# Kernel optimization log

Measured on AMD Instinct MI355X. Metric: run time of the kernel, lower is better.

The kernel has to match this reference:

```python
import jax, jax.numpy as jnp
import numpy as np

NUM_USERS = 100000
NUM_ITEMS = 50000
EMB_DIM = 64
NUM_EDGES = 2000000


def setup_inputs() -> dict:
    key = jax.random.key(0)
    k1, k2, k3, k4 = jax.random.split(key, 4)
    user_table = jax.random.normal(k1, (NUM_USERS, EMB_DIM), dtype=jnp.float32) * 0.1
    item_table = jax.random.normal(k2, (NUM_ITEMS, EMB_DIM), dtype=jnp.float32) * 0.1
    user_idx = jax.random.randint(k3, (NUM_EDGES,), 0, NUM_USERS, dtype=jnp.int32)
    item_idx = jax.random.randint(k4, (NUM_EDGES,), 0, NUM_ITEMS, dtype=jnp.int32)
    return {"user_table": user_table, "item_table": item_table,
            "user_idx": user_idx, "item_idx": item_idx, "num_layers": 3}


def reference(user_table, item_table, user_idx, item_idx, num_layers):
    """LightGCN-style k-hop propagation over a sparse bipartite user-item graph.

    A_hat[u,i] = 1/sqrt(deg_u * deg_i); emb_out = mean over hops 0..K of A_hat^k @ emb_0.
    Returns concatenated [num_users+num_items, d] embeddings (forward() then slices).
    """
    n_users, d = user_table.shape
    n_items = item_table.shape[0]
    ones = jnp.ones(user_idx.shape[0], dtype=user_table.dtype)
    deg_u = jax.ops.segment_sum(ones, user_idx, num_segments=n_users)
    deg_i = jax.ops.segment_sum(ones, item_idx, num_segments=n_items)
    deg_u = jnp.where(deg_u > 0, deg_u, 1.0)
    deg_i = jnp.where(deg_i > 0, deg_i, 1.0)
    # per-edge symmetric normalization coefficient [E]
    norm = jax.lax.rsqrt(deg_u[user_idx] * deg_i[item_idx])

    u, it = user_table, item_table
    acc_u, acc_i = u, it
    for _ in range(num_layers):
        # messages: item -> user and user -> item (gather + weighted scatter-add)
        msg_u = jax.ops.segment_sum(norm[:, None] * it[item_idx], user_idx, num_segments=n_users)
        msg_i = jax.ops.segment_sum(norm[:, None] * u[user_idx], item_idx, num_segments=n_items)
        u, it = msg_u, msg_i
        acc_u = acc_u + u
        acc_i = acc_i + it
    scale = 1.0 / (num_layers + 1)
    return jnp.concatenate([acc_u * scale, acc_i * scale], axis=0)
```

## Files before the change

### kernel.cpp

```cpp
#include <hip/hip_runtime.h>
#include <hip/hip_fp16.h>
#include <stdint.h>

#define NU 100000
#define NI 50000
#define NN (NU + NI)
#define DIM 64
#define NE 2000000
#define TOT (NN * DIM)

#define NBU 782
#define NBI 782
#define NBKT (NBU + NBI)
#define SCAP 3064
#define CGRP 25
#define NC 63
#define CCAP 67584

#define BEPT1 4
#define BCH1 (256 * BEPT1)
#define BG1 ((NE + BCH1 - 1) / BCH1)
#define KB2 17

typedef float f4v __attribute__((ext_vector_type(4)));
typedef float f2v __attribute__((ext_vector_type(2)));

__device__ __forceinline__ int bucket_r0(int b) {
    return (b < NBU) ? (b << 7) : (NU + ((b - NBU) << 6));
}


__global__ void bin1_kernel(const int* __restrict__ uidx, const int* __restrict__ iidx,
                            int* __restrict__ ccur, uint32_t* __restrict__ cstg) {
    __shared__ int cnt[NC];
    __shared__ int base[NC + 1];
    __shared__ int gbase[NC];
    __shared__ uint32_t rec[2 * BCH1];
    __shared__ uint8_t cid[2 * BCH1];
    int tid = threadIdx.x;
    for (int i = tid; i < NC; i += 256) cnt[i] = 0;
    __syncthreads();

    uint32_t pk[2 * BEPT1]; int cs[2 * BEPT1]; int rk[2 * BEPT1];
    int t0 = blockIdx.x * BCH1 + tid;
#pragma unroll
    for (int k = 0; k < BEPT1; ++k) {
        int e = t0 + k * 256;
        bool ok = e < NE;
        int u = ok ? __builtin_nontemporal_load(uidx + e) : 0;
        int itm = ok ? __builtin_nontemporal_load(iidx + e) : 0;
        int b = u >> 7; int c = b / 25; int f5 = b - c * 25;
        pk[2 * k] = ((uint32_t)f5 << 23) | ((uint32_t)(u & 127) << 16) | (uint32_t)itm;
        cs[2 * k] = ok ? c : -1;
        int b2 = NBU + (itm >> 6); int c2 = b2 / 25; int f52 = b2 - c2 * 25;
        pk[2 * k + 1] = ((uint32_t)f52 << 23) | ((uint32_t)(itm & 63) << 17) | (uint32_t)u;
        cs[2 * k + 1] = ok ? c2 : -1;
    }
#pragma unroll
    for (int k = 0; k < 2 * BEPT1; ++k)
        rk[k] = (cs[k] >= 0) ? atomicAdd(&cnt[cs[k]], 1) : 0;
    __syncthreads();
    if (tid == 0) {
        int s = 0;
        for (int i = 0; i < NC; ++i) { base[i] = s; s += cnt[i]; }
        base[NC] = s;
    }
    __syncthreads();
    for (int i = tid; i < NC; i += 256)
        if (cnt[i] > 0) gbase[i] = atomicAdd(&ccur[i], cnt[i]);
#pragma unroll
    for (int k = 0; k < 2 * BEPT1; ++k)
        if (cs[k] >= 0) {
            int p = base[cs[k]] + rk[k];
            rec[p] = pk[k];
            cid[p] = (uint8_t)cs[k];
        }
    __syncthreads();
    int T = base[NC];
    for (int p = tid; p < T; p += 256) {
        int c = cid[p];
        int pos = gbase[c] + (p - base[c]);
        if (pos < CCAP)
            __builtin_nontemporal_store(rec[p], cstg + (size_t)c * CCAP + pos);
    }
}

__global__ void bin2_kernel(const int* __restrict__ ccnt, const uint32_t* __restrict__ cstg,
                            int* __restrict__ bktcur, uint32_t* __restrict__ stg) {
    int c = blockIdx.x / KB2;
    int sl = blockIdx.x % KB2;
    int n = min(ccnt[c], CCAP);
    int lo = sl * 4096;
    if (lo >= n) return;
    int hi = min(lo + 4096, n);
    int m = hi - lo;
    __shared__ int cnt[CGRP];
    __shared__ int base[CGRP + 1];
    __shared__ int gbase[CGRP];
    __shared__ uint32_t rec[4096];
    int tid = threadIdx.x;
    if (tid < CGRP) cnt[tid] = 0;
    __syncthreads();

    uint32_t pk[16]; int fa[16]; int rk[16];
    const uint32_t* run = cstg + (size_t)c * CCAP + lo;
#pragma unroll
    for (int k = 0; k < 16; ++k) {
        int p = tid + k * 256;
        bool ok = p < m;
        uint32_t r = ok ? __builtin_nontemporal_load(run + p) : 0;
        pk[k] = r;
        fa[k] = ok ? (int)(r >> 23) : -1;
    }
#pragma unroll
    for (int k = 0; k < 16; ++k)
        rk[k] = (fa[k] >= 0) ? atomicAdd(&cnt[fa[k]], 1) : 0;
    __syncthreads();
    if (tid == 0) {
        int s = 0;
        for (int i = 0; i < CGRP; ++i) { base[i] = s; s += cnt[i]; }
        base[CGRP] = s;
    }
    __syncthreads();
    if (tid < CGRP && cnt[tid] > 0)
        gbase[tid] = atomicAdd(&bktcur[c * CGRP + tid], cnt[tid]);
#pragma unroll
    for (int k = 0; k < 16; ++k)
        if (fa[k] >= 0) rec[base[fa[k]] + rk[k]] = pk[k];
    __syncthreads();
    int T = base[CGRP];
    for (int p = tid; p < T; p += 256) {
        uint32_t r = rec[p];
        int f5 = r >> 23;
        int pos = gbase[f5] + (p - base[f5]);
        if (pos < SCAP)
            __builtin_nontemporal_store(r, stg + (size_t)(c * CGRP + f5) * SCAP + pos);
    }
}

__global__ void scanB_kernel(const int* __restrict__ bktcnt, int* __restrict__ bktbase) {
    __shared__ int partial[256];
    int tid = threadIdx.x;
    int loc[7];
    int s = 0;
#pragma unroll
    for (int k = 0; k < 7; ++k) {
        int i = tid * 7 + k;
        loc[k] = (i < NBKT) ? min(bktcnt[i], SCAP) : 0;
        s += loc[k];
    }
    partial[tid] = s;
    __syncthreads();
    for (int off = 1; off < 256; off <<= 1) {
        int v = (tid >= off) ? partial[tid - off] : 0;
        __syncthreads();
        partial[tid] += v;
        __syncthreads();
    }
    int excl = (tid == 0) ? 0 : partial[tid - 1];
#pragma unroll
    for (int k = 0; k < 7; ++k) {
        int i = tid * 7 + k;
        if (i < NBKT) { bktbase[i] = excl; excl += loc[k]; }
    }
    if (tid == 255) bktbase[NBKT] = partial[255];
}

__global__ void placeB2_kernel(const int* __restrict__ bktbase, const uint32_t* __restrict__ stg,
                               int* __restrict__ rowptr, float* __restrict__ rdeg,
                               float* __restrict__ irdeg, int* __restrict__ nbrs) {
    __shared__ int rowstart[129];
    __shared__ int rowcnt[128];
    __shared__ int outb[SCAP];
    int b = blockIdx.x;
    int tid = threadIdx.x;
    int r0 = bucket_r0(b);
    int r1 = (b < NBU) ? min(r0 + 128, NU) : min(r0 + 64, NN);
    int nrows = r1 - r0;
    int lo = bktbase[b];
    int n = bktbase[b + 1] - lo;
    if (tid < nrows) rowcnt[tid] = 0;
    __syncthreads();
    const uint32_t* run = stg + (size_t)b * SCAP;
    bool isU = b < NBU;
    for (int p = tid; p < n; p += 256) {
        uint32_t r = __builtin_nontemporal_load(run + p);
        int row = isU ? ((r >> 16) & 0x7F) : ((r >> 17) & 0x3F);
        atomicAdd(&rowcnt[row], 1);
    }
    __syncthreads();
    if (tid == 0) {
        int s = 0;
        for (int i = 0; i < nrows; ++i) { rowstart[i] = s; s += rowcnt[i]; }
        rowstart[nrows] = s;
    }
    __syncthreads();
    if (tid < nrows) {
        int d = rowcnt[tid];
        rowptr[r0 + tid] = lo + rowstart[tid];
        rdeg[r0 + tid] = (d > 0) ? rsqrtf((float)d) : 1.0f;
        irdeg[r0 + tid] = (d > 0) ? sqrtf((float)d) : 1.0f;
        rowcnt[tid] = 0;
    }
    if (b == NBKT - 1 && tid == 0) rowptr[NN] = lo + n;
    __syncthreads();
    for (int p = tid; p < n; p += 256) {
        uint32_t r = __builtin_nontemporal_load(run + p);
        int row = isU ? ((r >> 16) & 0x7F) : ((r >> 17) & 0x3F);
        int nbr = isU ? (NU + (int)(r & 0xFFFF)) : (int)(r & 0x1FFFF);
        int rk = atomicAdd(&rowcnt[row], 1);
        outb[rowstart[row] + rk] = nbr;
    }
    __syncthreads();
    for (int i = tid; i < n; i += 256)
        __builtin_nontemporal_store(outb[i], nbrs + lo + i);
}


__global__ void initsrc_kernel(const float* __restrict__ ut, const float* __restrict__ it,
                               const float* __restrict__ rdeg, __half* __restrict__ srcH) {
    int i = blockIdx.x * blockDim.x + threadIdx.x;
    const int NU4 = NU * DIM / 4;
    const int T4 = TOT / 4;
    if (i >= T4) return;
    float4 v = (i < NU4) ? ((const float4*)ut)[i] : ((const float4*)it)[i - NU4];
    float r = rdeg[i >> 4];
    union { __half2 h2[2]; f2v v2; } u;
    u.h2[0] = __floats2half2_rn(r * v.x, r * v.y);
    u.h2[1] = __floats2half2_rn(r * v.z, r * v.w);
    *((f2v*)(srcH + (size_t)i * 4)) = u.v2;
}

__device__ __forceinline__ void gather_core(const int* __restrict__ rowptr,
                                            const int* __restrict__ nbrs,
                                            const __half* __restrict__ srcH,
                                            int wid, int lane, int g, int c,
                                            float* out) {
    int start = rowptr[wid];
    int end = rowptr[wid + 1];
    int deg = end - start;
    int nb_l = (lane < deg) ? __builtin_nontemporal_load(nbrs + start + lane) : 0;
    float acc[4][8];
#pragma unroll
    for (int j = 0; j < 4; ++j)
#pragma unroll
        for (int k = 0; k < 8; ++k) acc[j][k] = 0.f;
    int dmain = deg < 64 ? deg : 64;
    int iters = (dmain + 7) >> 3;
    int t = 0;
    for (; t + 4 <= iters; t += 4) {
        int nb[4]; bool ok[4];
#pragma unroll
        for (int j = 0; j < 4; ++j) {
            int idx = (t + j) * 8 + g;
            nb[j] = __shfl(nb_l, idx & 63, 64);
            ok[j] = idx < dmain;
            if (!ok[j]) nb[j] = 0;
        }
        union { f4v v; __half2 h2[4]; } u[4];
#pragma unroll
        for (int j = 0; j < 4; ++j)
            u[j].v = *((const f4v*)(srcH + (size_t)nb[j] * DIM) + c);
#pragma unroll
        for (int j = 0; j < 4; ++j)
            if (ok[j]) {
#pragma unroll
                for (int h = 0; h < 4; ++h) {
                    float2 f = __half22float2(u[j].h2[h]);
                    acc[j][2 * h] += f.x; acc[j][2 * h + 1] += f.y;
                }
            }
    }
    if (t + 2 <= iters) {
        int nb[2]; bool ok[2];
#pragma unroll
        for (int j = 0; j < 2; ++j) {
            int idx = (t + j) * 8 + g;
            nb[j] = __shfl(nb_l, idx & 63, 64);
            ok[j] = idx < dmain;
            if (!ok[j]) nb[j] = 0;
        }
        union { f4v v; __half2 h2[4]; } u[2];
#pragma unroll
        for (int j = 0; j < 2; ++j)
            u[j].v = *((const f4v*)(srcH + (size_t)nb[j] * DIM) + c);
#pragma unroll
        for (int j = 0; j < 2; ++j)
            if (ok[j]) {
#pragma unroll
                for (int h = 0; h < 4; ++h) {
                    float2 f = __half22float2(u[j].h2[h]);
                    acc[j][2 * h] += f.x; acc[j][2 * h + 1] += f.y;
                }
            }
        t += 2;
    }
    if (t < iters) {
        int idx = t * 8 + g;
        int nb0 = __shfl(nb_l, idx & 63, 64);
        bool ok0 = idx < dmain;
        if (!ok0) nb0 = 0;
        union { f4v v; __half2 h2[4]; } u0;
        u0.v = *((const f4v*)(srcH + (size_t)nb0 * DIM) + c);
        if (ok0) {
#pragma unroll
            for (int h = 0; h < 4; ++h) {
                float2 f = __half22float2(u0.h2[h]);
                acc[0][2 * h] += f.x; acc[0][2 * h + 1] += f.y;
            }
        }
    }
    for (int k = start + 64 + g; k < end; k += 8) {
        int nb = nbrs[k];
        union { f4v v; __half2 h2[4]; } u0;
        u0.v = *((const f4v*)(srcH + (size_t)nb * DIM) + c);
#pragma unroll
        for (int h = 0; h < 4; ++h) {
            float2 f = __half22float2(u0.h2[h]);
            acc[0][2 * h] += f.x; acc[0][2 * h + 1] += f.y;
        }
    }
    float s[8];
#pragma unroll
    for (int k = 0; k < 8; ++k)
        s[k] = acc[0][k] + acc[1][k] + acc[2][k] + acc[3][k];
#pragma unroll
    for (int mask = 8; mask <= 32; mask <<= 1) {
#pragma unroll
        for (int k = 0; k < 8; ++k) s[k] += __shfl_xor(s[k], mask, 64);
    }
#pragma unroll
    for (int k = 0; k < 8; ++k) out[k] = s[k];
}

__global__ void gather_kernel(const int* __restrict__ rowptr, const int* __restrict__ nbrs,
                              const float* __restrict__ rdeg,
                              const __half* __restrict__ srcH, __half* __restrict__ nxtH) {
    int wid = (int)(((unsigned)blockIdx.x * blockDim.x + threadIdx.x) >> 6);
    if (wid >= NN) return;
    int lane = threadIdx.x & 63;
    int g = lane >> 3;
    int c = lane & 7;
    float s[8];
    gather_core(rowptr, nbrs, srcH, wid, lane, g, c, s);
    if (lane < 8) {
        float r = rdeg[wid];
        float w = r * r;
        union { f4v v; __half2 h2[4]; } o;
        o.h2[0] = __floats2half2_rn(w * s[0], w * s[1]);
        o.h2[1] = __floats2half2_rn(w * s[2], w * s[3]);
        o.h2[2] = __floats2half2_rn(w * s[4], w * s[5]);
        o.h2[3] = __floats2half2_rn(w * s[6], w * s[7]);
        __builtin_nontemporal_store(o.v, (f4v*)(nxtH + (size_t)wid * DIM + c * 8));
    }
}

__global__ void gather_fused_kernel(const int* __restrict__ rowptr, const int* __restrict__ nbrs,
                                    const float* __restrict__ rdeg, const float* __restrict__ irdeg,
                                    const __half* __restrict__ srcH,
                                    const __half* __restrict__ a0H, const __half* __restrict__ n1H,
                                    float* __restrict__ acc) {
    int wid = (int)(((unsigned)blockIdx.x * blockDim.x + threadIdx.x) >> 6);
    if (wid >= NN) return;
    int lane = threadIdx.x & 63;
    int g = lane >> 3;
    int c = lane & 7;
    float s[8];
    gather_core(rowptr, nbrs, srcH, wid, lane, g, c, s);
    if (lane < 8) {
        float r = rdeg[wid];
        float w = irdeg[wid];
        size_t ro = (size_t)wid * DIM + c * 8;
        union { f4v v; __half2 h2[4]; } a0, a1, a2;
        a0.v = __builtin_nontemporal_load((const f4v*)(a0H + ro));
        a1.v = __builtin_nontemporal_load((const f4v*)(n1H + ro));
        a2.v = *((const f4v*)(srcH + ro));
        f4v oa, ob;
        float2 e0 = __half22float2(a0.h2[0]), f1 = __half22float2(a1.h2[0]), f2 = __half22float2(a2.h2[0]);
        oa.x = 0.25f * (w * (e0.x + f1.x + f2.x) + r * s[0]);
        oa.y = 0.25f * (w * (e0.y + f1.y + f2.y) + r * s[1]);
        e0 = __half22float2(a0.h2[1]); f1 = __half22float2(a1.h2[1]); f2 = __half22float2(a2.h2[1]);
        oa.z = 0.25f * (w * (e0.x + f1.x + f2.x) + r * s[2]);
        oa.w = 0.25f * (w * (e0.y + f1.y + f2.y) + r * s[3]);
        e0 = __half22float2(a0.h2[2]); f1 = __half22float2(a1.h2[2]); f2 = __half22float2(a2.h2[2]);
        ob.x = 0.25f * (w * (e0.x + f1.x + f2.x) + r * s[4]);
        ob.y = 0.25f * (w * (e0.y + f1.y + f2.y) + r * s[5]);
        e0 = __half22float2(a0.h2[3]); f1 = __half22float2(a1.h2[3]); f2 = __half22float2(a2.h2[3]);
        ob.z = 0.25f * (w * (e0.x + f1.x + f2.x) + r * s[6]);
        ob.w = 0.25f * (w * (e0.y + f1.y + f2.y) + r * s[7]);
        __builtin_nontemporal_store(oa, (f4v*)(acc + ro));
        __builtin_nontemporal_store(ob, (f4v*)(acc + ro) + 1);
    }
}

extern "C" void kernel_launch(void* const* d_in, const int* in_sizes, int n_in,
                              void* d_out, int out_size, void* d_ws, size_t ws_size,
                              hipStream_t stream) {
    const float* ut = (const float*)d_in[0];
    const float* it = (const float*)d_in[1];
    const int* uidx = (const int*)d_in[2];
    const int* iidx = (const int*)d_in[3];

    float* acc = (float*)d_out;

    int* wsi = (int*)d_ws;
    int* rowptr = wsi;
    float* rdeg = (float*)(rowptr + (NN + 1));
    float* irdeg = rdeg + NN;
    int* bktcur = (int*)(irdeg + NN);
    int* ccur   = bktcur + NBKT;
    int* bktbase = ccur + NC;
    size_t off = (size_t)((int*)(bktbase + NBKT + 1) - wsi);
    off = (off + 15) & ~(size_t)15;
    int* nbrs   = wsi + off;
    __half* bufA = (__half*)(nbrs + 2 * (size_t)NE);
    __half* bufB = bufA + (size_t)TOT;
    __half* bufC = bufB + (size_t)TOT;
    uint32_t* stg  = (uint32_t*)bufA;
    uint32_t* cstg = (uint32_t*)bufB;

    const int B = 256;

    hipMemsetAsync(bktcur, 0, sizeof(int) * (NBKT + NC), stream);
    bin1_kernel<<<BG1, 256, 0, stream>>>(uidx, iidx, ccur, cstg);
    bin2_kernel<<<NC * KB2, 256, 0, stream>>>(ccur, cstg, bktcur, stg);
    scanB_kernel<<<1, 256, 0, stream>>>(bktcur, bktbase);
    placeB2_kernel<<<NBKT, 256, 0, stream>>>(bktbase, stg, rowptr, rdeg, irdeg, nbrs);

    initsrc_kernel<<<(TOT / 4 + B - 1) / B, B, 0, stream>>>(ut, it, rdeg, bufA);

    const int gblocks = NN / 4;
    gather_kernel<<<gblocks, B, 0, stream>>>(rowptr, nbrs, rdeg, bufA, bufB);
    gather_kernel<<<gblocks, B, 0, stream>>>(rowptr, nbrs, rdeg, bufB, bufC);
    gather_fused_kernel<<<gblocks, B, 0, stream>>>(rowptr, nbrs, rdeg, irdeg,
                                                   bufC, bufA, bufB, acc);
}
```

Measured before the change: 390.8 us.

## Fuse source init into CSR placement, sort neighbors, slim gather accumulators

The separate initsrc kernel is folded into placeB2: each bucket block now scales its own rows of the embedding tables by rsqrt(degree) and writes them as fp16. To make room, the staging buffer moves from bufA to bufC. Each row's neighbor list is also insertion-sorted in shared memory so gathers hit addresses in order, which should improve cache locality. Finally, the gather inner loop drops from four to two accumulator sets to cut register pressure. The price is a serial per-thread sort inside placement and less memory-level parallelism in the gather.

```diff
diff --git a/kernel.cpp b/kernel.cpp
--- a/kernel.cpp
+++ b/kernel.cpp
@@ -167,10 +167,13 @@
 }
 
 __global__ void placeB2_kernel(const int* __restrict__ bktbase, const uint32_t* __restrict__ stg,
+                               const float* __restrict__ ut, const float* __restrict__ it,
                                int* __restrict__ rowptr, float* __restrict__ rdeg,
-                               float* __restrict__ irdeg, int* __restrict__ nbrs) {
+                               float* __restrict__ irdeg, int* __restrict__ nbrs,
+                               __half* __restrict__ srcH) {
     __shared__ int rowstart[129];
     __shared__ int rowcnt[128];
+    __shared__ float rds[128];
     __shared__ int outb[SCAP];
     int b = blockIdx.x;
     int tid = threadIdx.x;
@@ -198,12 +201,27 @@
     if (tid < nrows) {
         int d = rowcnt[tid];
         rowptr[r0 + tid] = lo + rowstart[tid];
-        rdeg[r0 + tid] = (d > 0) ? rsqrtf((float)d) : 1.0f;
+        float rv = (d > 0) ? rsqrtf((float)d) : 1.0f;
+        rds[tid] = rv;
+        rdeg[r0 + tid] = rv;
         irdeg[r0 + tid] = (d > 0) ? sqrtf((float)d) : 1.0f;
         rowcnt[tid] = 0;
     }
     if (b == NBKT - 1 && tid == 0) rowptr[NN] = lo + n;
     __syncthreads();
+    {
+        const float* tbl = isU ? (ut + (size_t)r0 * DIM) : (it + (size_t)(r0 - NU) * DIM);
+        int nel4 = nrows * (DIM / 4);
+        f2v* dst = (f2v*)(srcH + (size_t)r0 * DIM);
+        for (int i = tid; i < nel4; i += 256) {
+            float4 v = ((const float4*)tbl)[i];
+            float rv = rds[i >> 4];
+            union { __half2 h2[2]; f2v v2; } u;
+            u.h2[0] = __floats2half2_rn(rv * v.x, rv * v.y);
+            u.h2[1] = __floats2half2_rn(rv * v.z, rv * v.w);
+            dst[i] = u.v2;
+        }
+    }
     for (int p = tid; p < n; p += 256) {
         uint32_t r = __builtin_nontemporal_load(run + p);
         int row = isU ? ((r >> 16) & 0x7F) : ((r >> 17) & 0x3F);
@@ -212,24 +230,20 @@
         outb[rowstart[row] + rk] = nbr;
     }
     __syncthreads();
+    if (tid < nrows) {
+        int s = rowstart[tid], e = rowstart[tid + 1];
+        for (int i = s + 1; i < e; ++i) {
+            int key = outb[i];
+            int j = i - 1;
+            while (j >= s && outb[j] > key) { outb[j + 1] = outb[j]; --j; }
+            outb[j + 1] = key;
+        }
+    }
+    __syncthreads();
     for (int i = tid; i < n; i += 256)
         __builtin_nontemporal_store(outb[i], nbrs + lo + i);
 }
 
-
-__global__ void initsrc_kernel(const float* __restrict__ ut, const float* __restrict__ it,
-                               const float* __restrict__ rdeg, __half* __restrict__ srcH) {
-    int i = blockIdx.x * blockDim.x + threadIdx.x;
-    const int NU4 = NU * DIM / 4;
-    const int T4 = TOT / 4;
-    if (i >= T4) return;
-    float4 v = (i < NU4) ? ((const float4*)ut)[i] : ((const float4*)it)[i - NU4];
-    float r = rdeg[i >> 4];
-    union { __half2 h2[2]; f2v v2; } u;
-    u.h2[0] = __floats2half2_rn(r * v.x, r * v.y);
-    u.h2[1] = __floats2half2_rn(r * v.z, r * v.w);
-    *((f2v*)(srcH + (size_t)i * 4)) = u.v2;
-}
 
 __device__ __forceinline__ void gather_core(const int* __restrict__ rowptr,
                                             const int* __restrict__ nbrs,
@@ -240,90 +254,61 @@
     int end = rowptr[wid + 1];
     int deg = end - start;
     int nb_l = (lane < deg) ? __builtin_nontemporal_load(nbrs + start + lane) : 0;
-    float acc[4][8];
-#pragma unroll
-    for (int j = 0; j < 4; ++j)
-#pragma unroll
-        for (int k = 0; k < 8; ++k) acc[j][k] = 0.f;
+    float s0=0,s1=0,s2=0,s3=0,s4=0,s5=0,s6=0,s7=0;
+    float q0=0,q1=0,q2=0,q3=0,q4=0,q5=0,q6=0,q7=0;
     int dmain = deg < 64 ? deg : 64;
     int iters = (dmain + 7) >> 3;
     int t = 0;
-    for (; t + 4 <= iters; t += 4) {
-        int nb[4]; bool ok[4];
-#pragma unroll
-        for (int j = 0; j < 4; ++j) {
-            int idx = (t + j) * 8 + g;
-            nb[j] = __shfl(nb_l, idx & 63, 64);
-            ok[j] = idx < dmain;
-            if (!ok[j]) nb[j] = 0;
-        }
-        union { f4v v; __half2 h2[4]; } u[4];
-#pragma unroll
-        for (int j = 0; j < 4; ++j)
-            u[j].v = *((const f4v*)(srcH + (size_t)nb[j] * DIM) + c);
-#pragma unroll
-        for (int j = 0; j < 4; ++j)
-            if (ok[j]) {
-#pragma unroll
-                for (int h = 0; h < 4; ++h) {
-                    float2 f = __half22float2(u[j].h2[h]);
-                    acc[j][2 * h] += f.x; acc[j][2 * h + 1] += f.y;
-                }
-            }
-    }
-    if (t + 2 <= iters) {
-        int nb[2]; bool ok[2];
-#pragma unroll
-        for (int j = 0; j < 2; ++j) {
-            int idx = (t + j) * 8 + g;
-            nb[j] = __shfl(nb_l, idx & 63, 64);
-            ok[j] = idx < dmain;
-            if (!ok[j]) nb[j] = 0;
-        }
-        union { f4v v; __half2 h2[4]; } u[2];
-#pragma unroll
-        for (int j = 0; j < 2; ++j)
-            u[j].v = *((const f4v*)(srcH + (size_t)nb[j] * DIM) + c);
-#pragma unroll
-        for (int j = 0; j < 2; ++j)
-            if (ok[j]) {
-#pragma unroll
-                for (int h = 0; h < 4; ++h) {
-                    float2 f = __half22float2(u[j].h2[h]);
-                    acc[j][2 * h] += f.x; acc[j][2 * h + 1] += f.y;
-                }
-            }
-        t += 2;
+    for (; t + 2 <= iters; t += 2) {
+        int idx0 = t * 8 + g;
+        int idx1 = idx0 + 8;
+        int nb0 = __shfl(nb_l, idx0, 64);
+        int nb1 = __shfl(nb_l, idx1, 64);
+        bool ok0 = idx0 < dmain, ok1 = idx1 < dmain;
+        if (!ok0) nb0 = 0;
+        if (!ok1) nb1 = 0;
+        union { f4v v; __half2 h2[4]; } u0, u1;
+        u0.v = *((const f4v*)(srcH + (size_t)nb0 * DIM) + c);
+        u1.v = *((const f4v*)(srcH + (size_t)nb1 * DIM) + c);
+        if (ok0) {
+            float2 f0 = __half22float2(u0.h2[0]), f1 = __half22float2(u0.h2[1]);
+            float2 f2 = __half22float2(u0.h2[2]), f3 = __half22float2(u0.h2[3]);
+            s0 += f0.x; s1 += f0.y; s2 += f1.x; s3 += f1.y;
+            s4 += f2.x; s5 += f2.y; s6 += f3.x; s7 += f3.y;
+        }
+        if (ok1) {
+            float2 f0 = __half22float2(u1.h2[0]), f1 = __half22float2(u1.h2[1]);
+            float2 f2 = __half22float2(u1.h2[2]), f3 = __half22float2(u1.h2[3]);
+            q0 += f0.x; q1 += f0.y; q2 += f1.x; q3 += f1.y;
+            q4 += f2.x; q5 += f2.y; q6 += f3.x; q7 += f3.y;
+        }
     }
     if (t < iters) {
-        int idx = t * 8 + g;
-        int nb0 = __shfl(nb_l, idx & 63, 64);
-        bool ok0 = idx < dmain;
+        int idx0 = t * 8 + g;
+        int nb0 = __shfl(nb_l, idx0, 64);
+        bool ok0 = idx0 < dmain;
         if (!ok0) nb0 = 0;
         union { f4v v; __half2 h2[4]; } u0;
         u0.v = *((const f4v*)(srcH + (size_t)nb0 * DIM) + c);
         if (ok0) {
-#pragma unroll
-            for (int h = 0; h < 4; ++h) {
-                float2 f = __half22float2(u0.h2[h]);
-                acc[0][2 * h] += f.x; acc[0][2 * h + 1] += f.y;
-            }
+            float2 f0 = __half22float2(u0.h2[0]), f1 = __half22float2(u0.h2[1]);
+            float2 f2 = __half22float2(u0.h2[2]), f3 = __half22float2(u0.h2[3]);
+            s0 += f0.x; s1 += f0.y; s2 += f1.x; s3 += f1.y;
+            s4 += f2.x; s5 += f2.y; s6 += f3.x; s7 += f3.y;
         }
     }
     for (int k = start + 64 + g; k < end; k += 8) {
         int nb = nbrs[k];
         union { f4v v; __half2 h2[4]; } u0;
         u0.v = *((const f4v*)(srcH + (size_t)nb * DIM) + c);
-#pragma unroll
-        for (int h = 0; h < 4; ++h) {
-            float2 f = __half22float2(u0.h2[h]);
-            acc[0][2 * h] += f.x; acc[0][2 * h + 1] += f.y;
-        }
-    }
-    float s[8];
-#pragma unroll
-    for (int k = 0; k < 8; ++k)
-        s[k] = acc[0][k] + acc[1][k] + acc[2][k] + acc[3][k];
+        float2 f0 = __half22float2(u0.h2[0]), f1 = __half22float2(u0.h2[1]);
+        float2 f2 = __half22float2(u0.h2[2]), f3 = __half22float2(u0.h2[3]);
+        s0 += f0.x; s1 += f0.y; s2 += f1.x; s3 += f1.y;
+        s4 += f2.x; s5 += f2.y; s6 += f3.x; s7 += f3.y;
+    }
+    s0 += q0; s1 += q1; s2 += q2; s3 += q3;
+    s4 += q4; s5 += q5; s6 += q6; s7 += q7;
+    float s[8] = {s0, s1, s2, s3, s4, s5, s6, s7};
 #pragma unroll
     for (int mask = 8; mask <= 32; mask <<= 1) {
 #pragma unroll
@@ -416,8 +401,8 @@
     __half* bufA = (__half*)(nbrs + 2 * (size_t)NE);
     __half* bufB = bufA + (size_t)TOT;
     __half* bufC = bufB + (size_t)TOT;
-    uint32_t* stg  = (uint32_t*)bufA;
     uint32_t* cstg = (uint32_t*)bufB;
+    uint32_t* stg  = (uint32_t*)bufC;
 
     const int B = 256;
 
@@ -425,9 +410,8 @@
     bin1_kernel<<<BG1, 256, 0, stream>>>(uidx, iidx, ccur, cstg);
     bin2_kernel<<<NC * KB2, 256, 0, stream>>>(ccur, cstg, bktcur, stg);
     scanB_kernel<<<1, 256, 0, stream>>>(bktcur, bktbase);
-    placeB2_kernel<<<NBKT, 256, 0, stream>>>(bktbase, stg, rowptr, rdeg, irdeg, nbrs);
-
-    initsrc_kernel<<<(TOT / 4 + B - 1) / B, B, 0, stream>>>(ut, it, rdeg, bufA);
+    placeB2_kernel<<<NBKT, 256, 0, stream>>>(bktbase, stg, ut, it,
+                                             rowptr, rdeg, irdeg, nbrs, bufA);
 
     const int gblocks = NN / 4;
     gather_kernel<<<gblocks, B, 0, stream>>>(rowptr, nbrs, rdeg, bufA, bufB);
```

After: 524.8 us. 1.34x slower.
